# Kernel optimization log

Measured on AMD Instinct MI355X. Metric: run time of the kernel, lower is better.

The kernel has to match this reference:

```python
import jax, jax.numpy as jnp
import numpy as np

DIM = 768
HEADS = 12
N_PATCH = 1024
ORDER = 5
DECAY = 0.5
EPS = 1e-6


def _exact_mask(N, order, decay):
    # 2D grid graph adjacency, row-major node order (matches sorted nx.grid_2d_graph nodes)
    side = int(np.sqrt(N))
    A = np.zeros((N, N), dtype=np.float64)
    idx = np.arange(N)
    r, c = idx // side, idx % side
    right = idx[c < side - 1]
    A[right, right + 1] = 1.0
    A[right + 1, right] = 1.0
    down = idx[r < side - 1]
    A[down, down + side] = 1.0
    A[down + side, down] = 1.0
    D_inv = 1.0 / np.maximum(A.sum(axis=1), 1.0)
    W = D_inv[:, None] * A
    M = np.eye(N)
    W_k = np.eye(N)
    coeff = 1.0
    for _ in range(order):
        W_k = W_k @ W
        coeff *= decay
        M += coeff * W_k
    M = M / M.sum(axis=1, keepdims=True)
    return jnp.asarray(M, dtype=jnp.float32)


def setup_inputs() -> dict:
    key = jax.random.key(0)
    k1, k2, k3, k4 = jax.random.split(key, 4)
    B = 4
    x = jax.random.normal(k1, (B, N_PATCH, DIM), dtype=jnp.float32)
    # nn.Linear(dim, 3*dim, bias=False): store as [dim, 3*dim] for x @ W
    scale = 1.0 / np.sqrt(DIM)
    W_qkv = jax.random.uniform(k2, (DIM, 3 * DIM), dtype=jnp.float32, minval=-scale, maxval=scale)
    W_out = jax.random.uniform(k3, (DIM, DIM), dtype=jnp.float32, minval=-scale, maxval=scale)
    b_out = jax.random.uniform(k4, (DIM,), dtype=jnp.float32, minval=-scale, maxval=scale)
    mask = _exact_mask(N_PATCH, ORDER, DECAY)
    return {"x": x, "W_qkv": W_qkv, "W_out": W_out, "b_out": b_out, "mask": mask}


def reference(x, W_qkv, W_out, b_out, mask):
    B, N, C = x.shape
    H, D = HEADS, C // HEADS
    qkv = x @ W_qkv  # [B, N, 3C]
    q, k, v = jnp.split(qkv, 3, axis=-1)
    # [B, N, C] -> [B, H, N, D]
    q, k, v = (t.reshape(B, N, H, D).transpose(0, 2, 1, 3) for t in (q, k, v))
    # feature map
    q = jax.nn.relu(q) + EPS
    k = jax.nn.relu(k) + EPS
    # (q^T @ M)^T = M^T @ q  ->  einsum over node axis
    q_graph = jnp.einsum('nm,bhnd->bhmd', mask, q)
    k_graph = jnp.einsum('nm,bhnd->bhmd', mask, k)
    q = q + 0.1 * q_graph
    k = k + 0.1 * k_graph
    linear_kernel = jnp.einsum('bhnd,bhmd->bhnm', q, k)  # [B, H, N, N]
    masked_kernel = linear_kernel * mask[None, None, :, :]
    z = 1.0 / (masked_kernel.sum(axis=-1, keepdims=True) + EPS)  # [B, H, N, 1]
    out = jnp.einsum('bhnm,bhmd->bhnd', masked_kernel, v) * z
    out = out.transpose(0, 2, 1, 3).reshape(B, N, C)
    return out @ W_out + b_out
```

## Files before the change

kernel.cpp:

```cpp
#include <hip/hip_runtime.h>

#define NP   1024
#define DIM  768
#define NH   12
#define HD   64
#define TQ   2304
#define EPS  1e-6f

typedef __attribute__((ext_vector_type(8))) short bf16x8;
typedef __attribute__((ext_vector_type(4))) float f32x4;

#define MFMA(a, b, c) __builtin_amdgcn_mfma_f32_16x16x32_bf16((a), (b), (c), 0, 0, 0)

__device__ __forceinline__ unsigned short f2b(float x) {
    unsigned int u = __builtin_bit_cast(unsigned int, x);
    u = (u + 0x7fffu + ((u >> 16) & 1u)) >> 16;
    return (unsigned short)u;
}
__device__ __forceinline__ float b2f(unsigned short h) {
    unsigned int u = ((unsigned int)h) << 16;
    return __builtin_bit_cast(float, u);
}
#if __has_builtin(__builtin_amdgcn_cvt_pk_bf16_f32)
typedef __attribute__((ext_vector_type(2))) __bf16 bf16x2t;
__device__ __forceinline__ unsigned int pk2(float lo, float hi) {
    bf16x2t v = __builtin_amdgcn_cvt_pk_bf16_f32(lo, hi);
    return __builtin_bit_cast(unsigned int, v);
}
#else
__device__ __forceinline__ unsigned int pk2(float lo, float hi) {
    return (unsigned int)f2b(lo) | ((unsigned int)f2b(hi) << 16);
}
#endif
__device__ __forceinline__ void gld16(const void* g, void* l) {
    __builtin_amdgcn_global_load_lds((const __attribute__((address_space(1))) unsigned int*)g,
                                     (__attribute__((address_space(3))) unsigned int*)l,
                                     16, 0, 0);
}

__device__ __forceinline__ void tile_transpose(const float* in, unsigned short* outp,
                                               int R, int C, int rt, int ct,
                                               bool isMask, float* buf ,
                                               int t ) {
    const int r0 = rt * 64, c0 = ct * 64;
    const int rr = t >> 4, cc = (t & 15) * 4;
    #pragma unroll
    for (int p = 0; p < 4; ++p) {
        float4 v = *(const float4*)(in + (size_t)(r0 + p * 16 + rr) * C + c0 + cc);
        buf[(p * 16 + rr) * 68 + cc + 0] = v.x; buf[(p * 16 + rr) * 68 + cc + 1] = v.y;
        buf[(p * 16 + rr) * 68 + cc + 2] = v.z; buf[(p * 16 + rr) * 68 + cc + 3] = v.w;
    }
    __syncthreads();
    const int oc = t >> 2, orr = (t & 3) * 16;
    alignas(16) unsigned short tmp[16];
    if (isMask) {
        #pragma unroll
        for (int j = 0; j < 16; ++j) {
            float v = 0.1f * buf[(orr + j) * 68 + oc] + ((c0 + oc) == (r0 + orr + j) ? 1.f : 0.f);
            tmp[j] = f2b(v);
        }
    } else {
        #pragma unroll
        for (int j = 0; j < 16; ++j) tmp[j] = f2b(buf[(orr + j) * 68 + oc]);
    }
    unsigned short* dst = outp + (size_t)(c0 + oc) * R + r0 + orr;
    *(uint4*)dst = *(const uint4*)tmp;
    *(uint4*)(dst + 8) = *(const uint4*)(tmp + 8);
}

__global__ __launch_bounds__(256) void k_prep1(const float* __restrict__ W_qkv,
                                               unsigned short* __restrict__ WqkvT) {
    __shared__ float buf[64 * 68];
    tile_transpose(W_qkv, WqkvT, 768, 2304, blockIdx.x / 36, blockIdx.x % 36,
                   false, buf, threadIdx.x);
}

__global__ __launch_bounds__(512) void k_gemm1(const float* __restrict__ X,
                                               const unsigned short* __restrict__ Bt,
                                               unsigned short* __restrict__ T,
                                               const float* __restrict__ W_out,
                                               const float* __restrict__ mask,
                                               unsigned short* __restrict__ WoutT,
                                               unsigned short* __restrict__ M2) {
    __shared__ __align__(16) unsigned char smem[34816];
    const int tid = threadIdx.x;
    const int bid = blockIdx.x;

    if (bid >= 576) {
        const int job = (bid - 576) * 2 + (tid >> 8);
        float* buf = (float*)(smem + (tid >> 8) * 17408);
        const int tt = tid & 255;
        if (job < 144) tile_transpose(W_out, WoutT, 768, 768, job / 12, job % 12, false, buf, tt);
        else { int j = job - 144; tile_transpose(mask, M2, 1024, 1024, j / 16, j % 16, true, buf, tt); }
        return;
    }

    unsigned short* As = (unsigned short*)smem;
    unsigned short* Bs = As + 2 * 128 * 32;
    const int w = tid >> 6, l = tid & 63;
    const int mstrip = (bid & 7) * 4 + ((bid >> 3) & 3);
    const int nstrip = bid >> 5;
    const int m0 = mstrip * 128, n0 = nstrip * 128;
    const int wm = (w & 3) * 32, wn = (w >> 2) * 64;
    const int quad = l >> 4, col = l & 15;
    const int lr = l >> 2, lc = (l & 3) * 8;
    const int arow = tid >> 2, akc = (tid & 3) * 8;

    f32x4 acc[2][4] = {};
    for (int k0 = 0; k0 < DIM; k0 += 64) {
        #pragma unroll
        for (int hh = 0; hh < 2; ++hh) {
            gld16(Bt + (size_t)(n0 + w * 16 + lr) * DIM + k0 + hh * 32 + lc,
                  Bs + (hh * 128 + w * 16) * 32);
            const float* xp = X + (size_t)(m0 + arow) * DIM + k0 + hh * 32 + akc;
            float4 xa = *(const float4*)xp;
            float4 xb = *(const float4*)(xp + 4);
            uint4 o;
            o.x = pk2(xa.x, xa.y); o.y = pk2(xa.z, xa.w);
            o.z = pk2(xb.x, xb.y); o.w = pk2(xb.z, xb.w);
            *(uint4*)(As + (hh * 128 + arow) * 32 + akc) = o;
        }
        __syncthreads();
        #pragma unroll
        for (int hh = 0; hh < 2; ++hh) {
            bf16x8 a[2], b[4];
            #pragma unroll
            for (int i = 0; i < 2; ++i)
                a[i] = *(const bf16x8*)(As + (hh * 128 + wm + i * 16 + col) * 32 + quad * 8);
            #pragma unroll
            for (int j = 0; j < 4; ++j)
                b[j] = *(const bf16x8*)(Bs + (hh * 128 + wn + j * 16 + col) * 32 + quad * 8);
            #pragma unroll
            for (int i = 0; i < 2; ++i)
                #pragma unroll
                for (int j = 0; j < 4; ++j)
                    acc[i][j] = MFMA(a[i], b[j], acc[i][j]);
        }
        __syncthreads();
    }

    const int cgb = n0 + wn;
    const int slot = cgb / DIM;
    const int h = (cgb % DIM) >> 6;
    const bool act = (slot < 2);
    const int sh = slot * 48 + (m0 >> 10) * NH + h;
    const int npb = (m0 & 1023) + wm + quad * 4;
    #pragma unroll
    for (int j = 0; j < 4; ++j) {
        unsigned short* dcol = T + ((size_t)(sh * HD + j * 16 + col)) * NP + npb;
        #pragma unroll
        for (int i = 0; i < 2; ++i) {
            float v0 = acc[i][j][0], v1 = acc[i][j][1], v2 = acc[i][j][2], v3 = acc[i][j][3];
            if (act) {
                v0 = fmaxf(v0, 0.f) + EPS; v1 = fmaxf(v1, 0.f) + EPS;
                v2 = fmaxf(v2, 0.f) + EPS; v3 = fmaxf(v3, 0.f) + EPS;
            }
            uint2 o; o.x = pk2(v0, v1); o.y = pk2(v2, v3);
            *(uint2*)(dcol + i * 16) = o;
        }
    }
}

__global__ __launch_bounds__(256) void k_graphmix(const unsigned short* __restrict__ M2,
                                                  const unsigned short* __restrict__ T,
                                                  unsigned short* __restrict__ q2) {
    const int bh = blockIdx.y, mt = blockIdx.x;
    const int m0 = mt * 64;
    __shared__ unsigned short M2s[4][64][32], Fq[4][64][32], Fk[4][64][32];
    const int tid = threadIdx.x, w = tid >> 6, l = tid & 63;
    const int quad = l >> 4, col = l & 15;
    const int lr = l >> 2, lc = (l & 3) * 8;
    const unsigned short* Tq = T + (size_t)bh * HD * NP;
    const unsigned short* Tk = T + (size_t)(48 + bh) * HD * NP;

    f32x4 accq[4] = {}, acck[4] = {};
    const int nr0 = min(max(2 * mt - 5, 0), 20) * 32;
    for (int it = 0; it < 3; ++it) {
        const int nc = nr0 + it * 128;
        __syncthreads();
        #pragma unroll
        for (int hh = 0; hh < 4; ++hh) {
            gld16(M2 + (size_t)(m0 + w * 16 + lr) * NP + nc + hh * 32 + lc, &M2s[hh][w * 16][0]);
            gld16(Tq + (size_t)(w * 16 + lr) * NP + nc + hh * 32 + lc, &Fq[hh][w * 16][0]);
            gld16(Tk + (size_t)(w * 16 + lr) * NP + nc + hh * 32 + lc, &Fk[hh][w * 16][0]);
        }
        __syncthreads();
        #pragma unroll
        for (int ks = 0; ks < 4; ++ks) {
            bf16x8 bm = *(const bf16x8*)&M2s[ks][w * 16 + col][quad * 8];
            #pragma unroll
            for (int dt = 0; dt < 4; ++dt) {
                bf16x8 aq = *(const bf16x8*)&Fq[ks][dt * 16 + col][quad * 8];
                bf16x8 ak = *(const bf16x8*)&Fk[ks][dt * 16 + col][quad * 8];
                accq[dt] = MFMA(aq, bm, accq[dt]);
                acck[dt] = MFMA(ak, bm, acck[dt]);
            }
        }
    }
    unsigned short* q2q = q2 + ((size_t)bh * NP + m0 + w * 16 + col) * HD;
    unsigned short* q2k = q2 + ((size_t)(48 + bh) * NP + m0 + w * 16 + col) * HD;
    #pragma unroll
    for (int dt = 0; dt < 4; ++dt) {
        const int d0 = dt * 16 + quad * 4;
        uint2 oq; oq.x = pk2(accq[dt][0], accq[dt][1]); oq.y = pk2(accq[dt][2], accq[dt][3]);
        uint2 ok; ok.x = pk2(acck[dt][0], acck[dt][1]); ok.y = pk2(acck[dt][2], acck[dt][3]);
        *(uint2*)(q2q + d0) = oq;
        *(uint2*)(q2k + d0) = ok;
    }
}

__global__ __launch_bounds__(256) void k_attn(const unsigned short* __restrict__ q2,
                                              const unsigned short* __restrict__ T,
                                              const float* __restrict__ mask,
                                              unsigned short* __restrict__ attnb) {
    const int bh = blockIdx.y, b = bh / NH, h = bh % NH;
    const int nt = blockIdx.x, n0 = nt * 64;
    __shared__ unsigned short Ks[2][2][64][32];
    __shared__ unsigned short VT[2][2][64][32];
    __shared__ unsigned int Ss2[2][32][68];
    __shared__ float rowz[64];
    const int tid = threadIdx.x, w = tid >> 6, l = tid & 63;
    const int quad = l >> 4, col = l & 15;
    const int lr = l >> 2, lc = (l & 3) * 8;

    const unsigned short* qb = q2 + ((size_t)bh * NP + n0) * HD;
    const unsigned short* kb = q2 + (size_t)(48 + bh) * NP * HD;
    const unsigned short* vtb = T + (size_t)(96 + bh) * HD * NP;

    bf16x8 aq[2];
    #pragma unroll
    for (int ks = 0; ks < 2; ++ks)
        aq[ks] = *(const bf16x8*)(qb + (size_t)(w * 16 + col) * HD + ks * 32 + quad * 8);

    f32x4 oacc[4] = {};
    float racc[4] = {};
    const int mr0 = min(max(2 * nt - 5, 0), 20) * 32;
    const unsigned int sel = (col & 1) ? 0x07060302u : 0x05040100u;

    for (int it3 = 0; it3 < 3; ++it3) {
        const int m0a = mr0 + it3 * 128;
        __syncthreads();
        #pragma unroll
        for (int t2 = 0; t2 < 2; ++t2)
            #pragma unroll
            for (int hh = 0; hh < 2; ++hh) {
                gld16(kb + (size_t)(m0a + t2 * 64 + w * 16 + lr) * HD + hh * 32 + lc,
                      &Ks[t2][hh][w * 16][0]);
                gld16(vtb + (size_t)(w * 16 + lr) * NP + m0a + t2 * 64 + hh * 32 + lc,
                      &VT[t2][hh][w * 16][0]);
            }
        float mreg[2][4][4];
        #pragma unroll
        for (int t2 = 0; t2 < 2; ++t2)
            #pragma unroll
            for (int mtt = 0; mtt < 4; ++mtt)
                #pragma unroll
                for (int r = 0; r < 4; ++r)
                    mreg[t2][mtt][r] = mask[(size_t)(n0 + w * 16 + quad * 4 + r) * NP
                                            + m0a + t2 * 64 + mtt * 16 + col];
        __syncthreads();

        #pragma unroll
        for (int t2 = 0; t2 < 2; ++t2) {
            f32x4 s[4] = {};
            #pragma unroll
            for (int ks = 0; ks < 2; ++ks)
                #pragma unroll
                for (int mtt = 0; mtt < 4; ++mtt) {
                    bf16x8 bk = *(const bf16x8*)&Ks[t2][ks][mtt * 16 + col][quad * 8];
                    s[mtt] = MFMA(aq[ks], bk, s[mtt]);
                }
            const int npr = w * 8 + quad * 2;
            #pragma unroll
            for (int mtt = 0; mtt < 4; ++mtt) {
                float v0 = s[mtt][0] * mreg[t2][mtt][0];
                float v1 = s[mtt][1] * mreg[t2][mtt][1];
                float v2 = s[mtt][2] * mreg[t2][mtt][2];
                float v3 = s[mtt][3] * mreg[t2][mtt][3];
                racc[0] += v0; racc[1] += v1; racc[2] += v2; racc[3] += v3;
                Ss2[t2][npr][mtt * 16 + col]     = pk2(v0, v1);
                Ss2[t2][npr + 1][mtt * 16 + col] = pk2(v2, v3);
            }
        }
        __syncthreads();

        #pragma unroll
        for (int t2 = 0; t2 < 2; ++t2)
            #pragma unroll
            for (int ks = 0; ks < 2; ++ks) {
                const unsigned int* rp = &Ss2[t2][w * 8 + (col >> 1)][ks * 32 + quad * 8];
                uint4 U  = *(const uint4*)rp;
                uint4 U2 = *(const uint4*)(rp + 4);
                uint4 fr;
                fr.x = __builtin_amdgcn_perm(U.y,  U.x,  sel);
                fr.y = __builtin_amdgcn_perm(U.w,  U.z,  sel);
                fr.z = __builtin_amdgcn_perm(U2.y, U2.x, sel);
                fr.w = __builtin_amdgcn_perm(U2.w, U2.z, sel);
                bf16x8 as = __builtin_bit_cast(bf16x8, fr);
                #pragma unroll
                for (int dt = 0; dt < 4; ++dt) {
                    bf16x8 bv = *(const bf16x8*)&VT[t2][ks][dt * 16 + col][quad * 8];
                    oacc[dt] = MFMA(as, bv, oacc[dt]);
                }
            }
    }

    #pragma unroll
    for (int r = 0; r < 4; ++r) {
        float v = racc[r];
        v += __shfl_xor(v, 1); v += __shfl_xor(v, 2);
        v += __shfl_xor(v, 4); v += __shfl_xor(v, 8);
        if (col == 0) rowz[w * 16 + quad * 4 + r] = v;
    }
    __syncthreads();
    #pragma unroll
    for (int r = 0; r < 4; ++r) {
        const int nl = w * 16 + quad * 4 + r;
        const float z = 1.f / (rowz[nl] + EPS);
        #pragma unroll
        for (int dt = 0; dt < 4; ++dt)
            attnb[(size_t)(b * NP + n0 + nl) * DIM + h * HD + dt * 16 + col] =
                f2b(oacc[dt][r] * z);
    }
}

__global__ __launch_bounds__(256) void k_gemm2(const unsigned short* __restrict__ A,
                                               const unsigned short* __restrict__ Bt,
                                               const float* __restrict__ bias,
                                               float* __restrict__ C) {
    __shared__ unsigned short As[2][64][32];
    __shared__ unsigned short Bs[2][64][32];
    const int tid = threadIdx.x, w = tid >> 6, l = tid & 63;
    const int bid = blockIdx.x;
    const int mstrip = (bid & 7) * 8 + ((bid >> 3) & 7);
    const int nstrip = bid >> 6;
    const int m0 = mstrip * 64, n0 = nstrip * 64;
    const int wm = (w & 1) * 32, wn = (w >> 1) * 32;
    const int quad = l >> 4, col = l & 15;
    const int lr = l >> 2, lc = (l & 3) * 8;

    f32x4 acc[2][2] = {};
    for (int k0 = 0; k0 < DIM; k0 += 64) {
        #pragma unroll
        for (int hh = 0; hh < 2; ++hh) {
            gld16(A + (size_t)(m0 + w * 16 + lr) * DIM + k0 + hh * 32 + lc, &As[hh][w * 16][0]);
            gld16(Bt + (size_t)(n0 + w * 16 + lr) * DIM + k0 + hh * 32 + lc, &Bs[hh][w * 16][0]);
        }
        __syncthreads();
        #pragma unroll
        for (int hh = 0; hh < 2; ++hh) {
            bf16x8 a[2], b[2];
            #pragma unroll
            for (int i = 0; i < 2; ++i) a[i] = *(const bf16x8*)&As[hh][wm + i * 16 + col][quad * 8];
            #pragma unroll
            for (int j = 0; j < 2; ++j) b[j] = *(const bf16x8*)&Bs[hh][wn + j * 16 + col][quad * 8];
            #pragma unroll
            for (int i = 0; i < 2; ++i)
                #pragma unroll
                for (int j = 0; j < 2; ++j)
                    acc[i][j] = MFMA(a[i], b[j], acc[i][j]);
        }
        __syncthreads();
    }
    #pragma unroll
    for (int i = 0; i < 2; ++i)
        #pragma unroll
        for (int j = 0; j < 2; ++j) {
            const int n = n0 + wn + j * 16 + col;
            #pragma unroll
            for (int r = 0; r < 4; ++r) {
                const int m = m0 + wm + i * 16 + quad * 4 + r;
                C[(size_t)m * DIM + n] = acc[i][j][r] + bias[n];
            }
        }
}

extern "C" void kernel_launch(void* const* d_in, const int* in_sizes, int n_in,
                              void* d_out, int out_size, void* d_ws, size_t ws_size,
                              hipStream_t stream) {
    (void)in_sizes; (void)n_in; (void)out_size; (void)ws_size;
    const float* x     = (const float*)d_in[0];
    const float* W_qkv = (const float*)d_in[1];
    const float* W_out = (const float*)d_in[2];
    const float* b_out = (const float*)d_in[3];
    const float* mask  = (const float*)d_in[4];
    float* out = (float*)d_out;

    unsigned short* p = (unsigned short*)d_ws;
    unsigned short* WqkvT = p; p += (size_t)TQ * DIM;
    unsigned short* WoutT = p; p += (size_t)DIM * DIM;
    unsigned short* M2    = p; p += (size_t)NP * NP;
    unsigned short* T     = p; p += (size_t)3 * 48 * HD * NP;
    unsigned short* q2    = p; p += (size_t)2 * 48 * NP * HD;
    unsigned short* attnb = p; p += (size_t)4096 * DIM;

    k_prep1<<<dim3(432), 256, 0, stream>>>(W_qkv, WqkvT);
    k_gemm1<<<dim3(776), 512, 0, stream>>>(x, WqkvT, T, W_out, mask, WoutT, M2);
    k_graphmix<<<dim3(NP / 64, 48), 256, 0, stream>>>(M2, T, q2);
    k_attn<<<dim3(NP / 64, 48), 256, 0, stream>>>(q2, T, mask, attnb);
    k_gemm2<<<dim3(768), 256, 0, stream>>>(attnb, WoutT, b_out, out);
}
```

Baseline: 155.0 us.

## Fuse all phases into one cooperative persistent kernel with grid syncs

Merges the five separate kernels into one cooperative kernel of 768 blocks that runs the prep, QKV GEMM, graph mix, attention and output GEMM phases, separated by grid-wide barriers. This is meant to remove per-launch overhead and the gaps between kernels. The QKV GEMM is also retiled from 128x128 tiles with 512 threads to 64x64 tiles with 256 threads, so it can share the fused block shape. A fallback to separate launches is kept in case the cooperative launch fails. The costs are grid-sync overhead, smaller and less efficient GEMM tiles, and a block residency requirement of 768 blocks, which relies on 3 blocks per CU fitting in LDS and registers.

```diff
diff --git a/kernel.cpp b/kernel.cpp
--- a/kernel.cpp
+++ b/kernel.cpp
@@ -1,4 +1,7 @@
 #include <hip/hip_runtime.h>
+#include <hip/hip_cooperative_groups.h>
+
+namespace cg = cooperative_groups;
 
 #define NP   1024
 #define DIM  768
@@ -17,10 +20,6 @@
     u = (u + 0x7fffu + ((u >> 16) & 1u)) >> 16;
     return (unsigned short)u;
 }
-__device__ __forceinline__ float b2f(unsigned short h) {
-    unsigned int u = ((unsigned int)h) << 16;
-    return __builtin_bit_cast(float, u);
-}
 #if __has_builtin(__builtin_amdgcn_cvt_pk_bf16_f32)
 typedef __attribute__((ext_vector_type(2))) __bf16 bf16x2t;
 __device__ __forceinline__ unsigned int pk2(float lo, float hi) {
@@ -38,17 +37,22 @@
                                      16, 0, 0);
 }
 
+struct P {
+    const float* X; const float* Wq; const float* Wo; const float* bo; const float* mk;
+    unsigned short* WqT; unsigned short* WoT; unsigned short* M2; unsigned short* T;
+    unsigned short* q2; unsigned short* attnb; float* out;
+};
+
 __device__ __forceinline__ void tile_transpose(const float* in, unsigned short* outp,
                                                int R, int C, int rt, int ct,
-                                               bool isMask, float* buf ,
-                                               int t ) {
+                                               bool isMask, float* buf , int t) {
     const int r0 = rt * 64, c0 = ct * 64;
     const int rr = t >> 4, cc = (t & 15) * 4;
     #pragma unroll
-    for (int p = 0; p < 4; ++p) {
-        float4 v = *(const float4*)(in + (size_t)(r0 + p * 16 + rr) * C + c0 + cc);
-        buf[(p * 16 + rr) * 68 + cc + 0] = v.x; buf[(p * 16 + rr) * 68 + cc + 1] = v.y;
-        buf[(p * 16 + rr) * 68 + cc + 2] = v.z; buf[(p * 16 + rr) * 68 + cc + 3] = v.w;
+    for (int pp = 0; pp < 4; ++pp) {
+        float4 v = *(const float4*)(in + (size_t)(r0 + pp * 16 + rr) * C + c0 + cc);
+        buf[(pp * 16 + rr) * 68 + cc + 0] = v.x; buf[(pp * 16 + rr) * 68 + cc + 1] = v.y;
+        buf[(pp * 16 + rr) * 68 + cc + 2] = v.z; buf[(pp * 16 + rr) * 68 + cc + 3] = v.w;
     }
     __syncthreads();
     const int oc = t >> 2, orr = (t & 3) * 16;
@@ -68,89 +72,67 @@
     *(uint4*)(dst + 8) = *(const uint4*)(tmp + 8);
 }
 
-__global__ __launch_bounds__(256) void k_prep1(const float* __restrict__ W_qkv,
-                                               unsigned short* __restrict__ WqkvT) {
-    __shared__ float buf[64 * 68];
-    tile_transpose(W_qkv, WqkvT, 768, 2304, blockIdx.x / 36, blockIdx.x % 36,
-                   false, buf, threadIdx.x);
-}
-
-__global__ __launch_bounds__(512) void k_gemm1(const float* __restrict__ X,
-                                               const unsigned short* __restrict__ Bt,
-                                               unsigned short* __restrict__ T,
-                                               const float* __restrict__ W_out,
-                                               const float* __restrict__ mask,
-                                               unsigned short* __restrict__ WoutT,
-                                               unsigned short* __restrict__ M2) {
-    __shared__ __align__(16) unsigned char smem[34816];
-    const int tid = threadIdx.x;
-    const int bid = blockIdx.x;
-
-    if (bid >= 576) {
-        const int job = (bid - 576) * 2 + (tid >> 8);
-        float* buf = (float*)(smem + (tid >> 8) * 17408);
-        const int tt = tid & 255;
-        if (job < 144) tile_transpose(W_out, WoutT, 768, 768, job / 12, job % 12, false, buf, tt);
-        else { int j = job - 144; tile_transpose(mask, M2, 1024, 1024, j / 16, j % 16, true, buf, tt); }
-        return;
-    }
-
+__device__ __forceinline__ void phase_prep(int j, int tid, unsigned char* smem, const P& p) {
+    float* buf = (float*)smem;
+    if (j < 432)      tile_transpose(p.Wq, p.WqT, 768, 2304, j / 36, j % 36, false, buf, tid);
+    else if (j < 576) { int q = j - 432; tile_transpose(p.Wo, p.WoT, 768, 768, q / 12, q % 12, false, buf, tid); }
+    else              { int q = j - 576; tile_transpose(p.mk, p.M2, 1024, 1024, q / 16, q % 16, true, buf, tid); }
+}
+
+__device__ __forceinline__ void phase_g1(int jj, int tid, unsigned char* smem, const P& p) {
     unsigned short* As = (unsigned short*)smem;
-    unsigned short* Bs = As + 2 * 128 * 32;
+    unsigned short* Bs = As + 4096;
     const int w = tid >> 6, l = tid & 63;
-    const int mstrip = (bid & 7) * 4 + ((bid >> 3) & 3);
-    const int nstrip = bid >> 5;
-    const int m0 = mstrip * 128, n0 = nstrip * 128;
-    const int wm = (w & 3) * 32, wn = (w >> 2) * 64;
+    const int mstrip = jj & 63, nstrip = jj >> 6;
+    const int m0 = mstrip * 64, n0 = nstrip * 64;
+    const int wm = (w & 1) * 32, wn = (w >> 1) * 32;
     const int quad = l >> 4, col = l & 15;
     const int lr = l >> 2, lc = (l & 3) * 8;
     const int arow = tid >> 2, akc = (tid & 3) * 8;
 
-    f32x4 acc[2][4] = {};
+    f32x4 acc[2][2] = {};
     for (int k0 = 0; k0 < DIM; k0 += 64) {
         #pragma unroll
         for (int hh = 0; hh < 2; ++hh) {
-            gld16(Bt + (size_t)(n0 + w * 16 + lr) * DIM + k0 + hh * 32 + lc,
-                  Bs + (hh * 128 + w * 16) * 32);
-            const float* xp = X + (size_t)(m0 + arow) * DIM + k0 + hh * 32 + akc;
+            gld16(p.WqT + (size_t)(n0 + w * 16 + lr) * DIM + k0 + hh * 32 + lc,
+                  Bs + (hh * 64 + w * 16) * 32);
+            const float* xp = p.X + (size_t)(m0 + arow) * DIM + k0 + hh * 32 + akc;
             float4 xa = *(const float4*)xp;
             float4 xb = *(const float4*)(xp + 4);
             uint4 o;
             o.x = pk2(xa.x, xa.y); o.y = pk2(xa.z, xa.w);
             o.z = pk2(xb.x, xb.y); o.w = pk2(xb.z, xb.w);
-            *(uint4*)(As + (hh * 128 + arow) * 32 + akc) = o;
+            *(uint4*)(As + (hh * 64 + arow) * 32 + akc) = o;
         }
         __syncthreads();
         #pragma unroll
         for (int hh = 0; hh < 2; ++hh) {
-            bf16x8 a[2], b[4];
+            bf16x8 a[2], b[2];
             #pragma unroll
             for (int i = 0; i < 2; ++i)
-                a[i] = *(const bf16x8*)(As + (hh * 128 + wm + i * 16 + col) * 32 + quad * 8);
-            #pragma unroll
-            for (int j = 0; j < 4; ++j)
-                b[j] = *(const bf16x8*)(Bs + (hh * 128 + wn + j * 16 + col) * 32 + quad * 8);
+                a[i] = *(const bf16x8*)(As + (hh * 64 + wm + i * 16 + col) * 32 + quad * 8);
+            #pragma unroll
+            for (int jx = 0; jx < 2; ++jx)
+                b[jx] = *(const bf16x8*)(Bs + (hh * 64 + wn + jx * 16 + col) * 32 + quad * 8);
             #pragma unroll
             for (int i = 0; i < 2; ++i)
                 #pragma unroll
-                for (int j = 0; j < 4; ++j)
-                    acc[i][j] = MFMA(a[i], b[j], acc[i][j]);
-        }
-        __syncthreads();
-    }
-
-    const int cgb = n0 + wn;
-    const int slot = cgb / DIM;
-    const int h = (cgb % DIM) >> 6;
+                for (int jx = 0; jx < 2; ++jx)
+                    acc[i][jx] = MFMA(a[i], b[jx], acc[i][jx]);
+        }
+        __syncthreads();
+    }
+    const int slot = n0 / DIM;
+    const int h = (n0 % DIM) >> 6;
     const bool act = (slot < 2);
     const int sh = slot * 48 + (m0 >> 10) * NH + h;
     const int npb = (m0 & 1023) + wm + quad * 4;
     #pragma unroll
-    for (int j = 0; j < 4; ++j) {
-        unsigned short* dcol = T + ((size_t)(sh * HD + j * 16 + col)) * NP + npb;
+    for (int jx = 0; jx < 2; ++jx) {
+        unsigned short* dcol = p.T + ((size_t)(sh * HD + wn + jx * 16 + col)) * NP + npb;
         #pragma unroll
         for (int i = 0; i < 2; ++i) {
-            float v0 = acc[i][j][0], v1 = acc[i][j][1], v2 = acc[i][j][2], v3 = acc[i][j][3];
+            float v0 = acc[i][jx][0], v1 = acc[i][jx][1], v2 = acc[i][jx][2], v3 = acc[i][jx][3];
             if (act) {
                 v0 = fmaxf(v0, 0.f) + EPS; v1 = fmaxf(v1, 0.f) + EPS;
                 v2 = fmaxf(v2, 0.f) + EPS; v3 = fmaxf(v3, 0.f) + EPS;
@@ -161,17 +143,17 @@
     }
 }
 
-__global__ __launch_bounds__(256) void k_graphmix(const unsigned short* __restrict__ M2,
-                                                  const unsigned short* __restrict__ T,
-                                                  unsigned short* __restrict__ q2) {
-    const int bh = blockIdx.y, mt = blockIdx.x;
+__device__ __forceinline__ void phase_gm(int bid, int tid, unsigned char* smem, const P& p) {
+    unsigned short* M2s = (unsigned short*)smem;
+    unsigned short* Fq = M2s + 8192;
+    unsigned short* Fk = Fq + 8192;
+    const int bh = bid >> 4, mt = bid & 15;
     const int m0 = mt * 64;
-    __shared__ unsigned short M2s[4][64][32], Fq[4][64][32], Fk[4][64][32];
-    const int tid = threadIdx.x, w = tid >> 6, l = tid & 63;
+    const int w = tid >> 6, l = tid & 63;
     const int quad = l >> 4, col = l & 15;
     const int lr = l >> 2, lc = (l & 3) * 8;
-    const unsigned short* Tq = T + (size_t)bh * HD * NP;
-    const unsigned short* Tk = T + (size_t)(48 + bh) * HD * NP;
+    const unsigned short* Tq = p.T + (size_t)bh * HD * NP;
+    const unsigned short* Tk = p.T + (size_t)(48 + bh) * HD * NP;
 
     f32x4 accq[4] = {}, acck[4] = {};
     const int nr0 = min(max(2 * mt - 5, 0), 20) * 32;
@@ -180,25 +162,25 @@
         __syncthreads();
         #pragma unroll
         for (int hh = 0; hh < 4; ++hh) {
-            gld16(M2 + (size_t)(m0 + w * 16 + lr) * NP + nc + hh * 32 + lc, &M2s[hh][w * 16][0]);
-            gld16(Tq + (size_t)(w * 16 + lr) * NP + nc + hh * 32 + lc, &Fq[hh][w * 16][0]);
-            gld16(Tk + (size_t)(w * 16 + lr) * NP + nc + hh * 32 + lc, &Fk[hh][w * 16][0]);
+            gld16(p.M2 + (size_t)(m0 + w * 16 + lr) * NP + nc + hh * 32 + lc, M2s + (hh * 64 + w * 16) * 32);
+            gld16(Tq + (size_t)(w * 16 + lr) * NP + nc + hh * 32 + lc, Fq + (hh * 64 + w * 16) * 32);
+            gld16(Tk + (size_t)(w * 16 + lr) * NP + nc + hh * 32 + lc, Fk + (hh * 64 + w * 16) * 32);
         }
         __syncthreads();
         #pragma unroll
         for (int ks = 0; ks < 4; ++ks) {
-            bf16x8 bm = *(const bf16x8*)&M2s[ks][w * 16 + col][quad * 8];
+            bf16x8 bm = *(const bf16x8*)(M2s + (ks * 64 + w * 16 + col) * 32 + quad * 8);
             #pragma unroll
             for (int dt = 0; dt < 4; ++dt) {
-                bf16x8 aq = *(const bf16x8*)&Fq[ks][dt * 16 + col][quad * 8];
-                bf16x8 ak = *(const bf16x8*)&Fk[ks][dt * 16 + col][quad * 8];
+                bf16x8 aq = *(const bf16x8*)(Fq + (ks * 64 + dt * 16 + col) * 32 + quad * 8);
+                bf16x8 ak = *(const bf16x8*)(Fk + (ks * 64 + dt * 16 + col) * 32 + quad * 8);
                 accq[dt] = MFMA(aq, bm, accq[dt]);
                 acck[dt] = MFMA(ak, bm, acck[dt]);
             }
         }
     }
-    unsigned short* q2q = q2 + ((size_t)bh * NP + m0 + w * 16 + col) * HD;
-    unsigned short* q2k = q2 + ((size_t)(48 + bh) * NP + m0 + w * 16 + col) * HD;
+    unsigned short* q2q = p.q2 + ((size_t)bh * NP + m0 + w * 16 + col) * HD;
+    unsigned short* q2k = p.q2 + ((size_t)(48 + bh) * NP + m0 + w * 16 + col) * HD;
     #pragma unroll
     for (int dt = 0; dt < 4; ++dt) {
         const int d0 = dt * 16 + quad * 4;
@@ -209,23 +191,21 @@
     }
 }
 
-__global__ __launch_bounds__(256) void k_attn(const unsigned short* __restrict__ q2,
-                                              const unsigned short* __restrict__ T,
-                                              const float* __restrict__ mask,
-                                              unsigned short* __restrict__ attnb) {
-    const int bh = blockIdx.y, b = bh / NH, h = bh % NH;
-    const int nt = blockIdx.x, n0 = nt * 64;
-    __shared__ unsigned short Ks[2][2][64][32];
-    __shared__ unsigned short VT[2][2][64][32];
-    __shared__ unsigned int Ss2[2][32][68];
-    __shared__ float rowz[64];
-    const int tid = threadIdx.x, w = tid >> 6, l = tid & 63;
+__device__ __forceinline__ void phase_at(int bid, int tid, unsigned char* smem, const P& p) {
+    unsigned short* Ks = (unsigned short*)smem;
+    unsigned short* VT = Ks + 8192;
+    unsigned int* Ss2 = (unsigned int*)(smem + 32768);
+    float* rowz = (float*)(smem + 32768 + 17408);
+    const int bh = bid >> 4, nt = bid & 15;
+    const int b = bh / NH, h = bh % NH;
+    const int n0 = nt * 64;
+    const int w = tid >> 6, l = tid & 63;
     const int quad = l >> 4, col = l & 15;
     const int lr = l >> 2, lc = (l & 3) * 8;
 
-    const unsigned short* qb = q2 + ((size_t)bh * NP + n0) * HD;
-    const unsigned short* kb = q2 + (size_t)(48 + bh) * NP * HD;
-    const unsigned short* vtb = T + (size_t)(96 + bh) * HD * NP;
+    const unsigned short* qb = p.q2 + ((size_t)bh * NP + n0) * HD;
+    const unsigned short* kb = p.q2 + (size_t)(48 + bh) * NP * HD;
+    const unsigned short* vtb = p.T + (size_t)(96 + bh) * HD * NP;
 
     bf16x8 aq[2];
     #pragma unroll
@@ -245,9 +225,9 @@
             #pragma unroll
             for (int hh = 0; hh < 2; ++hh) {
                 gld16(kb + (size_t)(m0a + t2 * 64 + w * 16 + lr) * HD + hh * 32 + lc,
-                      &Ks[t2][hh][w * 16][0]);
+                      Ks + ((t2 * 2 + hh) * 64 + w * 16) * 32);
                 gld16(vtb + (size_t)(w * 16 + lr) * NP + m0a + t2 * 64 + hh * 32 + lc,
-                      &VT[t2][hh][w * 16][0]);
+                      VT + ((t2 * 2 + hh) * 64 + w * 16) * 32);
             }
         float mreg[2][4][4];
         #pragma unroll
@@ -256,7 +236,7 @@
             for (int mtt = 0; mtt < 4; ++mtt)
                 #pragma unroll
                 for (int r = 0; r < 4; ++r)
-                    mreg[t2][mtt][r] = mask[(size_t)(n0 + w * 16 + quad * 4 + r) * NP
+                    mreg[t2][mtt][r] = p.mk[(size_t)(n0 + w * 16 + quad * 4 + r) * NP
                                             + m0a + t2 * 64 + mtt * 16 + col];
         __syncthreads();
 
@@ -267,7 +247,7 @@
             for (int ks = 0; ks < 2; ++ks)
                 #pragma unroll
                 for (int mtt = 0; mtt < 4; ++mtt) {
-                    bf16x8 bk = *(const bf16x8*)&Ks[t2][ks][mtt * 16 + col][quad * 8];
+                    bf16x8 bk = *(const bf16x8*)(Ks + ((t2 * 2 + ks) * 64 + mtt * 16 + col) * 32 + quad * 8);
                     s[mtt] = MFMA(aq[ks], bk, s[mtt]);
                 }
             const int npr = w * 8 + quad * 2;
@@ -278,8 +258,8 @@
                 float v2 = s[mtt][2] * mreg[t2][mtt][2];
                 float v3 = s[mtt][3] * mreg[t2][mtt][3];
                 racc[0] += v0; racc[1] += v1; racc[2] += v2; racc[3] += v3;
-                Ss2[t2][npr][mtt * 16 + col]     = pk2(v0, v1);
-                Ss2[t2][npr + 1][mtt * 16 + col] = pk2(v2, v3);
+                Ss2[(t2 * 32 + npr) * 68 + mtt * 16 + col]     = pk2(v0, v1);
+                Ss2[(t2 * 32 + npr + 1) * 68 + mtt * 16 + col] = pk2(v2, v3);
             }
         }
         __syncthreads();
@@ -288,7 +268,7 @@
         for (int t2 = 0; t2 < 2; ++t2)
             #pragma unroll
             for (int ks = 0; ks < 2; ++ks) {
-                const unsigned int* rp = &Ss2[t2][w * 8 + (col >> 1)][ks * 32 + quad * 8];
+                const unsigned int* rp = Ss2 + (t2 * 32 + w * 8 + (col >> 1)) * 68 + ks * 32 + quad * 8;
                 uint4 U  = *(const uint4*)rp;
                 uint4 U2 = *(const uint4*)(rp + 4);
                 uint4 fr;
@@ -299,7 +279,7 @@
                 bf16x8 as = __builtin_bit_cast(bf16x8, fr);
                 #pragma unroll
                 for (int dt = 0; dt < 4; ++dt) {
-                    bf16x8 bv = *(const bf16x8*)&VT[t2][ks][dt * 16 + col][quad * 8];
+                    bf16x8 bv = *(const bf16x8*)(VT + ((t2 * 2 + ks) * 64 + dt * 16 + col) * 32 + quad * 8);
                     oacc[dt] = MFMA(as, bv, oacc[dt]);
                 }
             }
@@ -319,21 +299,16 @@
         const float z = 1.f / (rowz[nl] + EPS);
         #pragma unroll
         for (int dt = 0; dt < 4; ++dt)
-            attnb[(size_t)(b * NP + n0 + nl) * DIM + h * HD + dt * 16 + col] =
+            p.attnb[(size_t)(b * NP + n0 + nl) * DIM + h * HD + dt * 16 + col] =
                 f2b(oacc[dt][r] * z);
     }
 }
 
-__global__ __launch_bounds__(256) void k_gemm2(const unsigned short* __restrict__ A,
-                                               const unsigned short* __restrict__ Bt,
-                                               const float* __restrict__ bias,
-                                               float* __restrict__ C) {
-    __shared__ unsigned short As[2][64][32];
-    __shared__ unsigned short Bs[2][64][32];
-    const int tid = threadIdx.x, w = tid >> 6, l = tid & 63;
-    const int bid = blockIdx.x;
-    const int mstrip = (bid & 7) * 8 + ((bid >> 3) & 7);
-    const int nstrip = bid >> 6;
+__device__ __forceinline__ void phase_g2(int bid, int tid, unsigned char* smem, const P& p) {
+    unsigned short* As = (unsigned short*)smem;
+    unsigned short* Bs = As + 4096;
+    const int w = tid >> 6, l = tid & 63;
+    const int mstrip = bid & 63, nstrip = bid >> 6;
     const int m0 = mstrip * 64, n0 = nstrip * 64;
     const int wm = (w & 1) * 32, wn = (w >> 1) * 32;
     const int quad = l >> 4, col = l & 15;
@@ -343,60 +318,111 @@
     for (int k0 = 0; k0 < DIM; k0 += 64) {
         #pragma unroll
         for (int hh = 0; hh < 2; ++hh) {
-            gld16(A + (size_t)(m0 + w * 16 + lr) * DIM + k0 + hh * 32 + lc, &As[hh][w * 16][0]);
-            gld16(Bt + (size_t)(n0 + w * 16 + lr) * DIM + k0 + hh * 32 + lc, &Bs[hh][w * 16][0]);
+            gld16(p.attnb + (size_t)(m0 + w * 16 + lr) * DIM + k0 + hh * 32 + lc,
+                  As + (hh * 64 + w * 16) * 32);
+            gld16(p.WoT + (size_t)(n0 + w * 16 + lr) * DIM + k0 + hh * 32 + lc,
+                  Bs + (hh * 64 + w * 16) * 32);
         }
         __syncthreads();
         #pragma unroll
         for (int hh = 0; hh < 2; ++hh) {
             bf16x8 a[2], b[2];
             #pragma unroll
-            for (int i = 0; i < 2; ++i) a[i] = *(const bf16x8*)&As[hh][wm + i * 16 + col][quad * 8];
-            #pragma unroll
-            for (int j = 0; j < 2; ++j) b[j] = *(const bf16x8*)&Bs[hh][wn + j * 16 + col][quad * 8];
+            for (int i = 0; i < 2; ++i)
+                a[i] = *(const bf16x8*)(As + (hh * 64 + wm + i * 16 + col) * 32 + quad * 8);
+            #pragma unroll
+            for (int jx = 0; jx < 2; ++jx)
+                b[jx] = *(const bf16x8*)(Bs + (hh * 64 + wn + jx * 16 + col) * 32 + quad * 8);
             #pragma unroll
             for (int i = 0; i < 2; ++i)
                 #pragma unroll
-                for (int j = 0; j < 2; ++j)
-                    acc[i][j] = MFMA(a[i], b[j], acc[i][j]);
+                for (int jx = 0; jx < 2; ++jx)
+                    acc[i][jx] = MFMA(a[i], b[jx], acc[i][jx]);
         }
         __syncthreads();
     }
     #pragma unroll
     for (int i = 0; i < 2; ++i)
         #pragma unroll
-        for (int j = 0; j < 2; ++j) {
-            const int n = n0 + wn + j * 16 + col;
+        for (int jx = 0; jx < 2; ++jx) {
+            const int n = n0 + wn + jx * 16 + col;
             #pragma unroll
             for (int r = 0; r < 4; ++r) {
                 const int m = m0 + wm + i * 16 + quad * 4 + r;
-                C[(size_t)m * DIM + n] = acc[i][j][r] + bias[n];
-            }
-        }
+                p.out[(size_t)m * DIM + n] = acc[i][jx][r] + p.bo[n];
+            }
+        }
+}
+
+__global__ __launch_bounds__(256, 3) void k_fused(P p) {
+    __shared__ __align__(16) unsigned char smem[50432];
+    cg::grid_group gg = cg::this_grid();
+    const int bid = blockIdx.x, tid = threadIdx.x;
+
+    for (int j = bid; j < 832; j += 768) {
+        if (j >= 768) __syncthreads();
+        phase_prep(j, tid, smem, p);
+    }
+    gg.sync();
+    for (int jj = bid; jj < 2304; jj += 768)
+        phase_g1(jj, tid, smem, p);
+    gg.sync();
+    phase_gm(bid, tid, smem, p);
+    gg.sync();
+    phase_at(bid, tid, smem, p);
+    gg.sync();
+    phase_g2(bid, tid, smem, p);
+}
+
+__global__ __launch_bounds__(256) void k_prep_s(P p) {
+    __shared__ __align__(16) unsigned char smem[17408];
+    phase_prep(blockIdx.x, threadIdx.x, smem, p);
+}
+__global__ __launch_bounds__(256) void k_g1_s(P p) {
+    __shared__ __align__(16) unsigned char smem[16384];
+    phase_g1(blockIdx.x, threadIdx.x, smem, p);
+}
+__global__ __launch_bounds__(256) void k_gm_s(P p) {
+    __shared__ __align__(16) unsigned char smem[49152];
+    phase_gm(blockIdx.x, threadIdx.x, smem, p);
+}
+__global__ __launch_bounds__(256) void k_at_s(P p) {
+    __shared__ __align__(16) unsigned char smem[50432];
+    phase_at(blockIdx.x, threadIdx.x, smem, p);
+}
+__global__ __launch_bounds__(256) void k_g2_s(P p) {
+    __shared__ __align__(16) unsigned char smem[16384];
+    phase_g2(blockIdx.x, threadIdx.x, smem, p);
 }
 
 extern "C" void kernel_launch(void* const* d_in, const int* in_sizes, int n_in,
                               void* d_out, int out_size, void* d_ws, size_t ws_size,
                               hipStream_t stream) {
     (void)in_sizes; (void)n_in; (void)out_size; (void)ws_size;
-    const float* x     = (const float*)d_in[0];
-    const float* W_qkv = (const float*)d_in[1];
-    const float* W_out = (const float*)d_in[2];
-    const float* b_out = (const float*)d_in[3];
-    const float* mask  = (const float*)d_in[4];
-    float* out = (float*)d_out;
-
-    unsigned short* p = (unsigned short*)d_ws;
-    unsigned short* WqkvT = p; p += (size_t)TQ * DIM;
-    unsigned short* WoutT = p; p += (size_t)DIM * DIM;
-    unsigned short* M2    = p; p += (size_t)NP * NP;
-    unsigned short* T     = p; p += (size_t)3 * 48 * HD * NP;
-    unsigned short* q2    = p; p += (size_t)2 * 48 * NP * HD;
-    unsigned short* attnb = p; p += (size_t)4096 * DIM;
-
-    k_prep1<<<dim3(432), 256, 0, stream>>>(W_qkv, WqkvT);
-    k_gemm1<<<dim3(776), 512, 0, stream>>>(x, WqkvT, T, W_out, mask, WoutT, M2);
-    k_graphmix<<<dim3(NP / 64, 48), 256, 0, stream>>>(M2, T, q2);
-    k_attn<<<dim3(NP / 64, 48), 256, 0, stream>>>(q2, T, mask, attnb);
-    k_gemm2<<<dim3(768), 256, 0, stream>>>(attnb, WoutT, b_out, out);
-}
+    unsigned short* q = (unsigned short*)d_ws;
+    P p;
+    p.X  = (const float*)d_in[0];
+    p.Wq = (const float*)d_in[1];
+    p.Wo = (const float*)d_in[2];
+    p.bo = (const float*)d_in[3];
+    p.mk = (const float*)d_in[4];
+    p.out = (float*)d_out;
+    p.WqT   = q; q += (size_t)TQ * DIM;
+    p.WoT   = q; q += (size_t)DIM * DIM;
+    p.M2    = q; q += (size_t)NP * NP;
+    p.T     = q; q += (size_t)3 * 48 * HD * NP;
+    p.q2    = q; q += (size_t)2 * 48 * NP * HD;
+    p.attnb = q; q += (size_t)4096 * DIM;
+
+    void* args[] = {(void*)&p};
+    hipError_t e = hipLaunchCooperativeKernel((const void*)k_fused, dim3(768), dim3(256),
+                                              args, 0, stream);
+    if (e != hipSuccess) {
+        (void)hipGetLastError();
+        k_prep_s<<<dim3(832), 256, 0, stream>>>(p);
+        k_g1_s<<<dim3(2304), 256, 0, stream>>>(p);
+        k_gm_s<<<dim3(768), 256, 0, stream>>>(p);
+        k_at_s<<<dim3(768), 256, 0, stream>>>(p);
+        k_g2_s<<<dim3(768), 256, 0, stream>>>(p);
+    }
+}
```

Result: slower. 566.5 us (+265.6%).
